# Optimization experiments

Measured on AMD Instinct MI355X. Metric: run time of the kernel, lower is better.

Reference implementation:

```python
import jax, jax.numpy as jnp
import numpy as np
import math

B, S, H = 2, 2048, 1024
NH, HD = 16, 64
MAX_SCALE = 4


def setup_inputs() -> dict:
    key = jax.random.key(0)
    ks = jax.random.split(key, 8)
    s = 0.02
    return {
        "x": jax.random.normal(ks[0], (B, S, H), dtype=jnp.float32),
        "Wqkv": jax.random.normal(ks[1], (H, 3 * H), dtype=jnp.float32) * s,
        "bqkv": jnp.zeros((3 * H,), dtype=jnp.float32),
        "Wout": jax.random.normal(ks[2], (H, H), dtype=jnp.float32) * s,
        "bout": jnp.zeros((H,), dtype=jnp.float32),
        "Wscale": jax.random.normal(ks[3], (H, MAX_SCALE), dtype=jnp.float32) * s,
        "bscale": jnp.zeros((MAX_SCALE,), dtype=jnp.float32),
    }


def reference(x, Wqkv, bqkv, Wout, bout, Wscale, bscale):
    b, s, h = x.shape
    inv_sqrt_hd = 1.0 / math.sqrt(HD)
    # qkv projection -> [3, b, nh, s, hd]
    qkv = (x @ Wqkv + bqkv).reshape(b, s, 3, NH, HD).transpose(2, 0, 3, 1, 4)
    q, k, v = qkv[0], qkv[1], qkv[2]
    # per-token soft weights over scales [b, s, max_scale]
    scale_weights = jax.nn.softmax(x @ Wscale + bscale, axis=-1)
    out = jnp.zeros((b, NH, s, HD), dtype=x.dtype)
    for scale_idx in range(MAX_SCALE):
        dilation = 2 ** scale_idx
        kd = k[:, :, ::dilation]  # strided (dilated) gather of keys
        vd = v[:, :, ::dilation]
        scores = jnp.einsum("bhqd,bhkd->bhqk", q, kd) * inv_sqrt_hd
        attn = jax.nn.softmax(scores, axis=-1)
        o = jnp.einsum("bhqk,bhkd->bhqd", attn, vd)
        w = scale_weights[:, :, scale_idx][:, None, :, None]  # [b,1,s,1]
        out = out + o * w
    out = out.transpose(0, 2, 1, 3).reshape(b, s, h)
    return out @ Wout + bout
```

## Files before the change

kernel.cpp:

```cpp
#include <hip/hip_runtime.h>
#include <stdint.h>

typedef unsigned short u16;
typedef __attribute__((ext_vector_type(8))) __bf16 bf8v;
typedef __attribute__((ext_vector_type(4))) float f4v;
typedef __attribute__((ext_vector_type(16))) float f16v;

#define BB 2
#define SS 2048
#define HH 1024

#define OFF_Q   0u
#define OFF_K0  8388608u
#define OFF_K1  16777216u
#define OFF_K2  20971520u
#define OFF_K3  23068672u
#define OFF_V0  24117248u
#define OFF_V1  32505856u
#define OFF_V2  36700160u
#define OFF_V3  38797312u
#define OFF_WQT 39845888u
#define OFF_WOT 46137344u
#define OFF_XB  48234496u
#define OFF_SCW 56623104u

__device__ __forceinline__ u16 f2bf(float f) {
    union { float f; uint32_t u; } v; v.f = f;
    uint32_t r = v.u + 0x7fffu + ((v.u >> 16) & 1u);
    return (u16)(r >> 16);
}
__device__ __forceinline__ uint32_t pk2(float a, float b) {
    return (uint32_t)f2bf(a) | ((uint32_t)f2bf(b) << 16);
}
__device__ __forceinline__ uint32_t pkt2(float a, float b) {
    union { float f; uint32_t u; } x, y; x.f = a; y.f = b;
    return (x.u >> 16) | (y.u & 0xffff0000u);
}
__device__ __forceinline__ u16 f2bft(float f) {
    union { float f; uint32_t u; } v; v.f = f;
    return (u16)(v.u >> 16);
}

__global__ __launch_bounds__(256) void xconv_kernel(const float* __restrict__ x,
                                                    u16* __restrict__ xb) {
    size_t t = (size_t)blockIdx.x * 256 + threadIdx.x;
    float4 v = *(const float4*)&x[t * 4];
    uint2 pk; pk.x = pk2(v.x, v.y); pk.y = pk2(v.z, v.w);
    *(uint2*)&xb[t * 4] = pk;
}

__global__ __launch_bounds__(256) void wconv_kernel(const float* __restrict__ W,
                                                    u16* __restrict__ Wt,
                                                    int N, int K) {
    __shared__ float tile[64][69];
    const int tid = threadIdx.x;
    const int n0 = blockIdx.x * 64, k0 = blockIdx.y * 64;
    const int r = tid >> 4, c4 = (tid & 15) * 4;
#pragma unroll
    for (int it = 0; it < 4; it++) {
        float4 v = *(const float4*)&W[(size_t)(k0 + it * 16 + r) * N + n0 + c4];
        tile[it * 16 + r][c4 + 0] = v.x; tile[it * 16 + r][c4 + 1] = v.y;
        tile[it * 16 + r][c4 + 2] = v.z; tile[it * 16 + r][c4 + 3] = v.w;
    }
    __syncthreads();
#pragma unroll
    for (int it = 0; it < 4; it++) {
        int n = it * 16 + r;
        uint2 pk;
        pk.x = pk2(tile[c4 + 0][n], tile[c4 + 1][n]);
        pk.y = pk2(tile[c4 + 2][n], tile[c4 + 3][n]);
        *(uint2*)&Wt[(size_t)(n0 + n) * K + k0 + c4] = pk;
    }
}

__global__ __launch_bounds__(256) void scale_kernel(const float* __restrict__ x,
                                                    const float* __restrict__ Wscale,
                                                    const float* __restrict__ bscale,
                                                    float* __restrict__ scw) {
    const int lane = threadIdx.x & 63;
    const int wid  = threadIdx.x >> 6;
    const int row  = blockIdx.x * 4 + wid;
    float a0 = 0.f, a1 = 0.f, a2 = 0.f, a3 = 0.f;
    for (int i = 0; i < 16; i++) {
        int hh = lane + i * 64;
        float xs = x[(size_t)row * HH + hh];
        float4 wv = *(const float4*)&Wscale[hh * 4];
        a0 += xs * wv.x; a1 += xs * wv.y; a2 += xs * wv.z; a3 += xs * wv.w;
    }
    for (int off = 1; off < 64; off <<= 1) {
        a0 += __shfl_xor(a0, off); a1 += __shfl_xor(a1, off);
        a2 += __shfl_xor(a2, off); a3 += __shfl_xor(a3, off);
    }
    if (lane == 0) {
        a0 += bscale[0]; a1 += bscale[1]; a2 += bscale[2]; a3 += bscale[3];
        float mx = fmaxf(fmaxf(a0, a1), fmaxf(a2, a3));
        float e0 = __expf(a0 - mx), e1 = __expf(a1 - mx);
        float e2 = __expf(a2 - mx), e3 = __expf(a3 - mx);
        float inv = 1.f / (e0 + e1 + e2 + e3);
        float4 o = {e0 * inv, e1 * inv, e2 * inv, e3 * inv};
        *(float4*)&scw[(size_t)row * 4] = o;
    }
}

template<int MODE>
__global__ __launch_bounds__(256) void gemm_bt(const u16* __restrict__ A,
                                               const u16* __restrict__ Bt,
                                               const float* __restrict__ bias,
                                               void* __restrict__ Cp,
                                               int N, int K) {
    __shared__ __align__(16) u16 At[128 * 40];
    __shared__ __align__(16) u16 Btl[128 * 40];
    const int tid  = threadIdx.x;
    const int lane = tid & 63;
    const int wid  = tid >> 6;
    const int l15  = lane & 15;
    const int quad = lane >> 4;
    const int wm = wid & 1, wn = wid >> 1;
    const int m0 = blockIdx.y * 128;
    const int n0 = blockIdx.x * 128;
    const int srow = tid >> 2;
    const int sc8  = (tid & 3) * 8;

    f4v acc[4][4];
#pragma unroll
    for (int i = 0; i < 4; i++)
#pragma unroll
        for (int j = 0; j < 4; j++) acc[i][j] = (f4v){0.f, 0.f, 0.f, 0.f};

    uint4 pa0 = *(const uint4*)(A  + (size_t)(m0 + srow) * K + sc8);
    uint4 pa1 = *(const uint4*)(A  + (size_t)(m0 + srow + 64) * K + sc8);
    uint4 pb0 = *(const uint4*)(Bt + (size_t)(n0 + srow) * K + sc8);
    uint4 pb1 = *(const uint4*)(Bt + (size_t)(n0 + srow + 64) * K + sc8);

    for (int kc = 0; kc < K; kc += 32) {
        __syncthreads();
        *(uint4*)&At[srow * 40 + sc8]         = pa0;
        *(uint4*)&At[(srow + 64) * 40 + sc8]  = pa1;
        *(uint4*)&Btl[srow * 40 + sc8]        = pb0;
        *(uint4*)&Btl[(srow + 64) * 40 + sc8] = pb1;
        __syncthreads();
        if (kc + 32 < K) {
            pa0 = *(const uint4*)(A  + (size_t)(m0 + srow) * K + kc + 32 + sc8);
            pa1 = *(const uint4*)(A  + (size_t)(m0 + srow + 64) * K + kc + 32 + sc8);
            pb0 = *(const uint4*)(Bt + (size_t)(n0 + srow) * K + kc + 32 + sc8);
            pb1 = *(const uint4*)(Bt + (size_t)(n0 + srow + 64) * K + kc + 32 + sc8);
        }
        bf8v af[4], bf[4];
#pragma unroll
        for (int t = 0; t < 4; t++) {
            af[t] = *(const bf8v*)&At[(wm * 64 + t * 16 + l15) * 40 + quad * 8];
            bf[t] = *(const bf8v*)&Btl[(wn * 64 + t * 16 + l15) * 40 + quad * 8];
        }
#pragma unroll
        for (int ti = 0; ti < 4; ti++)
#pragma unroll
            for (int tj = 0; tj < 4; tj++)
                acc[ti][tj] = __builtin_amdgcn_mfma_f32_16x16x32_bf16(af[ti], bf[tj], acc[ti][tj], 0, 0, 0);
    }

    if (MODE == 0) {
#pragma unroll
        for (int ti = 0; ti < 4; ti++)
#pragma unroll
            for (int tj = 0; tj < 4; tj++)
#pragma unroll
                for (int r = 0; r < 4; r++) {
                    int m = m0 + wm * 64 + ti * 16 + quad * 4 + r;
                    int n = n0 + wn * 64 + tj * 16 + l15;
                    ((float*)Cp)[(size_t)m * N + n] = acc[ti][tj][r] + bias[n];
                }
    } else {
        char* ws = (char*)Cp;
        u16* Qd = (u16*)ws;
        u16* K0 = (u16*)(ws + OFF_K0);
        u16* V0 = (u16*)(ws + OFF_V0); u16* V1 = (u16*)(ws + OFF_V1);
        u16* V2 = (u16*)(ws + OFF_V2); u16* V3 = (u16*)(ws + OFF_V3);
        const int region = n0 >> 10;
        if (region == 0) {
#pragma unroll
            for (int ti = 0; ti < 4; ti++)
#pragma unroll
                for (int tj = 0; tj < 4; tj++)
#pragma unroll
                    for (int r = 0; r < 4; r++) {
                        int m = m0 + wm * 64 + ti * 16 + quad * 4 + r;
                        int n = n0 + wn * 64 + tj * 16 + l15;
                        Qd[(size_t)m * 1024 + n] = f2bf(acc[ti][tj][r] + bias[n]);
                    }
        } else if (region == 1) {
#pragma unroll
            for (int ti = 0; ti < 4; ti++)
#pragma unroll
                for (int tj = 0; tj < 4; tj++) {
                    int n  = n0 + wn * 64 + tj * 16 + l15;
                    int nk = n - 1024;
                    int h = nk >> 6, hd = nk & 63;
#pragma unroll
                    for (int r = 0; r < 4; r++) {
                        int m = m0 + wm * 64 + ti * 16 + quad * 4 + r;
                        int bb = m >> 11, tok = m & 2047;
                        int bh = bb * 16 + h;
                        u16 bv = f2bf((acc[ti][tj][r] + bias[n]) * 0.18033688f);
                        K0[((size_t)bh * 2048 + tok) * 64 + hd] = bv;
                    }
                }
        } else {
#pragma unroll
            for (int ti = 0; ti < 4; ti++)
#pragma unroll
                for (int tj = 0; tj < 4; tj++) {
                    int n  = n0 + wn * 64 + tj * 16 + l15;
                    int nv = n - 2048;
                    int h = nv >> 6, hd = nv & 63;
                    int tokb = m0 + wm * 64 + ti * 16 + quad * 4;
                    int bb = tokb >> 11, tok = tokb & 2047;
                    int bh = bb * 16 + h;
                    float v0 = acc[ti][tj][0] + bias[n];
                    float v1 = acc[ti][tj][1] + bias[n];
                    float v2 = acc[ti][tj][2] + bias[n];
                    float v3 = acc[ti][tj][3] + bias[n];
                    u16 c0 = f2bf(v0), c1 = f2bf(v1), c2 = f2bf(v2), c3 = f2bf(v3);
                    uint2 pk;
                    pk.x = (uint32_t)c0 | ((uint32_t)c1 << 16);
                    pk.y = (uint32_t)c2 | ((uint32_t)c3 << 16);
                    *(uint2*)&V0[((size_t)bh * 64 + hd) * 2048 + tok] = pk;
                    *(uint32_t*)&V1[((size_t)bh * 64 + hd) * 1024 + (tok >> 1)] =
                        (uint32_t)c0 | ((uint32_t)c2 << 16);
                    V2[((size_t)bh * 64 + hd) * 512 + (tok >> 2)] = c0;
                    if (!(quad & 1)) V3[((size_t)bh * 64 + hd) * 256 + (tok >> 3)] = c0;
                }
        }
    }
}

__global__ __launch_bounds__(256, 2) void attn_kernel(const char* __restrict__ ws) {
    __shared__ __align__(16) u16 smem[30208];
    u16* Kt0  = smem;
    u16* Kt1  = smem + 2304;
    u16* Vt0  = smem + 4608;
    u16* Vt1  = smem + 7168;
    u16* V1t0 = smem + 9728;
    u16* V1t1 = smem + 11264;
    u16* V2t  = smem + 12800;
    u16* V3t  = smem + 14336;

    const u16* Qd    = (const u16*)(ws + OFF_Q);
    const float* scw = (const float*)(ws + OFF_SCW);
    u16* attnb       = (u16*)(ws + OFF_Q);

    const int tid  = threadIdx.x;
    const int lane = tid & 63;
    const int wid  = tid >> 6;
    const int l31  = lane & 31;
    const int half = lane >> 5;
    const int b = blockIdx.z, h = blockIdx.y;
    const int q  = blockIdx.x * 128 + wid * 32 + l31;
    const int bh = b * 16 + h;

    u16* Pw0 = smem + 15872 + wid * 3584;
    u16* Pwe = Pw0 + 1280;
    u16* Pw2 = Pwe + 768;
    u16* Pw3 = Pw2 + 768;

    const int skey = tid >> 3;
    const int shd8 = (tid & 7) * 8;
    const int svhd = tid >> 2;
    const int svk8 = (tid & 3) * 8;
    const int vi4  = (tid & 3) * 4;

    bf8v qf[4];
#pragma unroll
    for (int ks = 0; ks < 4; ks++)
        qf[ks] = *(const bf8v*)(Qd + (size_t)(b * SS + q) * 1024 + h * 64 + ks * 16 + half * 8);

    const u16* Kb  = (const u16*)(ws + OFF_K0) + (size_t)bh * (2048 * 64);
    const u16* Vb0 = (const u16*)(ws + OFF_V0) + (size_t)bh * (64 * 2048);
    const u16* Vb1 = (const u16*)(ws + OFF_V1) + (size_t)bh * (64 * 1024);
    const u16* Vb2 = (const u16*)(ws + OFF_V2) + (size_t)bh * (64 * 512);
    const u16* Vb3 = (const u16*)(ws + OFF_V3) + (size_t)bh * (64 * 256);

    f16v oacc0[2], oacc1[2], oacc2[2], oacc3[2];
#pragma unroll
    for (int ht = 0; ht < 2; ht++)
#pragma unroll
        for (int r = 0; r < 16; r++) {
            oacc0[ht][r] = 0.f; oacc1[ht][r] = 0.f;
            oacc2[ht][r] = 0.f; oacc3[ht][r] = 0.f;
        }
    float ls0 = 0.f, ls1 = 0.f, ls2 = 0.f, ls3 = 0.f;

    uint4 kr  = *(const uint4*)(Kb + (size_t)skey * 64 + shd8);
    uint4 vr  = *(const uint4*)(Vb0 + (size_t)svhd * 2048 + svk8);
    uint2 v1r = *(const uint2*)(Vb1 + (size_t)svhd * 1024 + vi4);
    uint2 v2r = *(const uint2*)(Vb2 + (size_t)svhd * 512 + vi4);
    uint2 v3r = *(const uint2*)(Vb3 + (size_t)svhd * 256 + vi4);
    *(uint4*)&Kt0[skey * 72 + shd8] = kr;
    *(uint4*)&Vt0[svhd * 40 + svk8] = vr;
    *(uint2*)&V1t0[svhd * 24 + vi4] = v1r;
    kr  = *(const uint4*)(Kb + (size_t)(32 + skey) * 64 + shd8);
    vr  = *(const uint4*)(Vb0 + (size_t)svhd * 2048 + 32 + svk8);
    v1r = *(const uint2*)(Vb1 + (size_t)svhd * 1024 + 16 + vi4);
    __syncthreads();

    for (int c = 0; c < 64; c++) {
        u16* Ktc  = (c & 1) ? Kt1 : Kt0;
        u16* Vtc  = (c & 1) ? Vt1 : Vt0;
        u16* V1tc = (c & 1) ? V1t1 : V1t0;
        u16* Ktn  = (c & 1) ? Kt0 : Kt1;
        u16* Vtn  = (c & 1) ? Vt0 : Vt1;
        u16* V1tn = (c & 1) ? V1t0 : V1t1;

        f16v sa;
#pragma unroll
        for (int r = 0; r < 16; r++) sa[r] = 0.f;
#pragma unroll
        for (int ks = 0; ks < 4; ks++) {
            bf8v ka = *(const bf8v*)&Ktc[l31 * 72 + ks * 16 + half * 8];
            sa = __builtin_amdgcn_mfma_f32_32x32x16_bf16(ka, qf[ks], sa, 0, 0, 0);
        }
#pragma unroll
        for (int g = 0; g < 4; g++) {
            float e0 = exp2f(sa[g * 4 + 0]);
            float e1 = exp2f(sa[g * 4 + 1]);
            float e2 = exp2f(sa[g * 4 + 2]);
            float e3 = exp2f(sa[g * 4 + 3]);
            ls0 += (e0 + e1) + (e2 + e3);
            ls1 += e0 + e2;
            ls2 += e0;
            if (!half) ls3 += e0;
            uint2 pk;
            pk.x = pkt2(e0, e1);
            pk.y = pkt2(e2, e3);
            *(uint2*)&Pw0[l31 * 40 + g * 8 + half * 4] = pk;
            *(uint32_t*)&Pwe[l31 * 24 + g * 4 + half * 2] = pkt2(e0, e2);
            Pw2[l31 * 24 + (c & 1) * 8 + g * 2 + half] = f2bft(e0);
            if (!half) Pw3[l31 * 24 + (c & 3) * 4 + g] = f2bft(e0);
        }
        if (c + 1 < 64) {
            *(uint4*)&Ktn[skey * 72 + shd8] = kr;
            *(uint4*)&Vtn[svhd * 40 + svk8] = vr;
            *(uint2*)&V1tn[svhd * 24 + vi4] = v1r;
        }
        if (!(c & 1)) {
            *(uint2*)&V2t[svhd * 24 + vi4] = v2r;
            if (!(c & 3))
                *(uint2*)&V3t[svhd * 24 + vi4] = v3r;
        }
        if (c + 2 < 64) {
            kr  = *(const uint4*)(Kb + (size_t)((c + 2) * 32 + skey) * 64 + shd8);
            vr  = *(const uint4*)(Vb0 + (size_t)svhd * 2048 + (c + 2) * 32 + svk8);
            v1r = *(const uint2*)(Vb1 + (size_t)svhd * 1024 + (c + 2) * 16 + vi4);
            if (!((c + 2) & 1))
                v2r = *(const uint2*)(Vb2 + (size_t)svhd * 512 + (c + 2) * 8 + vi4);
            if (!((c + 2) & 3))
                v3r = *(const uint2*)(Vb3 + (size_t)svhd * 256 + (c + 2) * 4 + vi4);
        }
        __asm__ volatile("s_waitcnt lgkmcnt(0)" ::: "memory");
#pragma unroll
        for (int kst = 0; kst < 2; kst++) {
            bf8v pb = *(const bf8v*)&Pw0[l31 * 40 + kst * 16 + half * 8];
#pragma unroll
            for (int ht = 0; ht < 2; ht++) {
                bf8v va = *(const bf8v*)&Vtc[(ht * 32 + l31) * 40 + kst * 16 + half * 8];
                oacc0[ht] = __builtin_amdgcn_mfma_f32_32x32x16_bf16(va, pb, oacc0[ht], 0, 0, 0);
            }
        }
        {
            bf8v pb1 = *(const bf8v*)&Pwe[l31 * 24 + half * 8];
#pragma unroll
            for (int ht = 0; ht < 2; ht++) {
                bf8v va1 = *(const bf8v*)&V1tc[(ht * 32 + l31) * 24 + half * 8];
                oacc1[ht] = __builtin_amdgcn_mfma_f32_32x32x16_bf16(va1, pb1, oacc1[ht], 0, 0, 0);
            }
        }
        if (c & 1) {
            bf8v pb2 = *(const bf8v*)&Pw2[l31 * 24 + half * 8];
#pragma unroll
            for (int ht = 0; ht < 2; ht++) {
                bf8v va2 = *(const bf8v*)&V2t[(ht * 32 + l31) * 24 + half * 8];
                oacc2[ht] = __builtin_amdgcn_mfma_f32_32x32x16_bf16(va2, pb2, oacc2[ht], 0, 0, 0);
            }
        }
        if ((c & 3) == 3) {
            bf8v pb3 = *(const bf8v*)&Pw3[l31 * 24 + half * 8];
#pragma unroll
            for (int ht = 0; ht < 2; ht++) {
                bf8v va3 = *(const bf8v*)&V3t[(ht * 32 + l31) * 24 + half * 8];
                oacc3[ht] = __builtin_amdgcn_mfma_f32_32x32x16_bf16(va3, pb3, oacc3[ht], 0, 0, 0);
            }
        }
        __syncthreads();
    }
    ls0 += __shfl_xor(ls0, 32);
    ls1 += __shfl_xor(ls1, 32);
    ls2 += __shfl_xor(ls2, 32);
    ls3 += __shfl_xor(ls3, 32);
    float4 sw = *(const float4*)&scw[(size_t)(b * SS + q) * 4];
    float w0 = sw.x / ls0, w1 = sw.y / ls1, w2 = sw.z / ls2, w3 = sw.w / ls3;

    const size_t base = (size_t)(b * SS + q) * 1024 + h * 64;
#pragma unroll
    for (int ht = 0; ht < 2; ht++)
#pragma unroll
        for (int g = 0; g < 4; g++) {
            float f0 = w0 * oacc0[ht][g * 4 + 0] + w1 * oacc1[ht][g * 4 + 0]
                     + w2 * oacc2[ht][g * 4 + 0] + w3 * oacc3[ht][g * 4 + 0];
            float f1 = w0 * oacc0[ht][g * 4 + 1] + w1 * oacc1[ht][g * 4 + 1]
                     + w2 * oacc2[ht][g * 4 + 1] + w3 * oacc3[ht][g * 4 + 1];
            float f2 = w0 * oacc0[ht][g * 4 + 2] + w1 * oacc1[ht][g * 4 + 2]
                     + w2 * oacc2[ht][g * 4 + 2] + w3 * oacc3[ht][g * 4 + 2];
            float f3 = w0 * oacc0[ht][g * 4 + 3] + w1 * oacc1[ht][g * 4 + 3]
                     + w2 * oacc2[ht][g * 4 + 3] + w3 * oacc3[ht][g * 4 + 3];
            uint2 pk;
            pk.x = pk2(f0, f1);
            pk.y = pk2(f2, f3);
            *(uint2*)&attnb[base + ht * 32 + g * 8 + half * 4] = pk;
        }
}

extern "C" void kernel_launch(void* const* d_in, const int* in_sizes, int n_in,
                              void* d_out, int out_size, void* d_ws, size_t ws_size,
                              hipStream_t stream) {
    const float* x      = (const float*)d_in[0];
    const float* Wqkv   = (const float*)d_in[1];
    const float* bqkv   = (const float*)d_in[2];
    const float* Wout   = (const float*)d_in[3];
    const float* bout   = (const float*)d_in[4];
    const float* Wscale = (const float*)d_in[5];
    const float* bscale = (const float*)d_in[6];
    float* out = (float*)d_out;

    char* ws = (char*)d_ws;
    u16*   wqt   = (u16*)(ws + OFF_WQT);
    u16*   wot   = (u16*)(ws + OFF_WOT);
    u16*   xb    = (u16*)(ws + OFF_XB);
    u16*   attnb = (u16*)(ws + OFF_Q);
    float* scw   = (float*)(ws + OFF_SCW);

    xconv_kernel<<<dim3(4096), dim3(256), 0, stream>>>(x, xb);
    wconv_kernel<<<dim3(48, 16), dim3(256), 0, stream>>>(Wqkv, wqt, 3072, 1024);
    wconv_kernel<<<dim3(16, 16), dim3(256), 0, stream>>>(Wout, wot, 1024, 1024);
    scale_kernel<<<dim3(1024), dim3(256), 0, stream>>>(x, Wscale, bscale, scw);
    gemm_bt<1><<<dim3(24, 32), dim3(256), 0, stream>>>(xb, wqt, bqkv, (void*)ws, 3072, 1024);
    attn_kernel<<<dim3(16, 16, 2), dim3(256), 0, stream>>>(ws);
    gemm_bt<0><<<dim3(8, 32), dim3(256), 0, stream>>>(attnb, wot, bout, (void*)out, 1024, 1024);
}
```

Measured before the change: 266.8 us.

## Keep softmax probabilities in registers by permuting V layout to match MFMA fragments

The probability tiles are no longer round-tripped through shared memory. The exp results are packed directly into bf16 MFMA B-operand registers. To make that legal, the QKV epilogue writes V0/V1/V2 with a permuted token order that matches the register fragment layout, and the scale-3 operand is assembled with a cross-half shuffle. The loop is unrolled by four so phase-dependent buffer choices become compile-time. This cuts LDS traffic and the lgkmcnt wait, and halves shared memory per block, which may raise occupancy. The cost is subtle index permutations that must match the MFMA lane mapping exactly.

```diff
diff --git a/kernel.cpp b/kernel.cpp
--- a/kernel.cpp
+++ b/kernel.cpp
@@ -5,6 +5,7 @@
 typedef __attribute__((ext_vector_type(8))) __bf16 bf8v;
 typedef __attribute__((ext_vector_type(4))) float f4v;
 typedef __attribute__((ext_vector_type(16))) float f16v;
+typedef __attribute__((ext_vector_type(4))) uint32_t u32x4;
 
 #define BB 2
 #define SS 2048
@@ -12,9 +13,6 @@
 
 #define OFF_Q   0u
 #define OFF_K0  8388608u
-#define OFF_K1  16777216u
-#define OFF_K2  20971520u
-#define OFF_K3  23068672u
 #define OFF_V0  24117248u
 #define OFF_V1  32505856u
 #define OFF_V2  36700160u
@@ -35,10 +33,6 @@
 __device__ __forceinline__ uint32_t pkt2(float a, float b) {
     union { float f; uint32_t u; } x, y; x.f = a; y.f = b;
     return (x.u >> 16) | (y.u & 0xffff0000u);
-}
-__device__ __forceinline__ u16 f2bft(float f) {
-    union { float f; uint32_t u; } v; v.f = f;
-    return (u16)(v.u >> 16);
 }
 
 __global__ __launch_bounds__(256) void xconv_kernel(const float* __restrict__ x,
@@ -223,10 +217,15 @@
                     uint2 pk;
                     pk.x = (uint32_t)c0 | ((uint32_t)c1 << 16);
                     pk.y = (uint32_t)c2 | ((uint32_t)c3 << 16);
-                    *(uint2*)&V0[((size_t)bh * 64 + hd) * 2048 + tok] = pk;
-                    *(uint32_t*)&V1[((size_t)bh * 64 + hd) * 1024 + (tok >> 1)] =
+                    int tokp = (tok & ~15) | ((tok & 4) << 1) | ((tok & 8) >> 1);
+                    *(uint2*)&V0[((size_t)bh * 64 + hd) * 2048 + tokp] = pk;
+                    int kk = tok >> 1;
+                    int v1p = (kk & ~15) | ((kk & 2) << 2) | ((kk & 12) >> 1);
+                    *(uint32_t*)&V1[((size_t)bh * 64 + hd) * 1024 + v1p] =
                         (uint32_t)c0 | ((uint32_t)c2 << 16);
-                    V2[((size_t)bh * 64 + hd) * 512 + (tok >> 2)] = c0;
+                    int t2 = tok >> 2;
+                    int v2i = (t2 & ~15) | ((t2 & 1) << 3) | ((t2 & 15) >> 1);
+                    V2[((size_t)bh * 64 + hd) * 512 + v2i] = c0;
                     if (!(quad & 1)) V3[((size_t)bh * 64 + hd) * 256 + (tok >> 3)] = c0;
                 }
         }
@@ -234,7 +233,7 @@
 }
 
 __global__ __launch_bounds__(256, 2) void attn_kernel(const char* __restrict__ ws) {
-    __shared__ __align__(16) u16 smem[30208];
+    __shared__ __align__(16) u16 smem[15872];
     u16* Kt0  = smem;
     u16* Kt1  = smem + 2304;
     u16* Vt0  = smem + 4608;
@@ -256,11 +255,6 @@
     const int b = blockIdx.z, h = blockIdx.y;
     const int q  = blockIdx.x * 128 + wid * 32 + l31;
     const int bh = b * 16 + h;
-
-    u16* Pw0 = smem + 15872 + wid * 3584;
-    u16* Pwe = Pw0 + 1280;
-    u16* Pw2 = Pwe + 768;
-    u16* Pw3 = Pw2 + 768;
 
     const int skey = tid >> 3;
     const int shd8 = (tid & 7) * 8;
@@ -302,94 +296,118 @@
     v1r = *(const uint2*)(Vb1 + (size_t)svhd * 1024 + 16 + vi4);
     __syncthreads();
 
-    for (int c = 0; c < 64; c++) {
-        u16* Ktc  = (c & 1) ? Kt1 : Kt0;
-        u16* Vtc  = (c & 1) ? Vt1 : Vt0;
-        u16* V1tc = (c & 1) ? V1t1 : V1t0;
-        u16* Ktn  = (c & 1) ? Kt0 : Kt1;
-        u16* Vtn  = (c & 1) ? Vt0 : Vt1;
-        u16* V1tn = (c & 1) ? V1t0 : V1t1;
-
-        f16v sa;
-#pragma unroll
-        for (int r = 0; r < 16; r++) sa[r] = 0.f;
-#pragma unroll
-        for (int ks = 0; ks < 4; ks++) {
-            bf8v ka = *(const bf8v*)&Ktc[l31 * 72 + ks * 16 + half * 8];
-            sa = __builtin_amdgcn_mfma_f32_32x32x16_bf16(ka, qf[ks], sa, 0, 0, 0);
-        }
-#pragma unroll
-        for (int g = 0; g < 4; g++) {
-            float e0 = exp2f(sa[g * 4 + 0]);
-            float e1 = exp2f(sa[g * 4 + 1]);
-            float e2 = exp2f(sa[g * 4 + 2]);
-            float e3 = exp2f(sa[g * 4 + 3]);
-            ls0 += (e0 + e1) + (e2 + e3);
-            ls1 += e0 + e2;
-            ls2 += e0;
-            if (!half) ls3 += e0;
-            uint2 pk;
-            pk.x = pkt2(e0, e1);
-            pk.y = pkt2(e2, e3);
-            *(uint2*)&Pw0[l31 * 40 + g * 8 + half * 4] = pk;
-            *(uint32_t*)&Pwe[l31 * 24 + g * 4 + half * 2] = pkt2(e0, e2);
-            Pw2[l31 * 24 + (c & 1) * 8 + g * 2 + half] = f2bft(e0);
-            if (!half) Pw3[l31 * 24 + (c & 3) * 4 + g] = f2bft(e0);
-        }
-        if (c + 1 < 64) {
-            *(uint4*)&Ktn[skey * 72 + shd8] = kr;
-            *(uint4*)&Vtn[svhd * 40 + svk8] = vr;
-            *(uint2*)&V1tn[svhd * 24 + vi4] = v1r;
-        }
-        if (!(c & 1)) {
-            *(uint2*)&V2t[svhd * 24 + vi4] = v2r;
-            if (!(c & 3))
-                *(uint2*)&V3t[svhd * 24 + vi4] = v3r;
-        }
-        if (c + 2 < 64) {
-            kr  = *(const uint4*)(Kb + (size_t)((c + 2) * 32 + skey) * 64 + shd8);
-            vr  = *(const uint4*)(Vb0 + (size_t)svhd * 2048 + (c + 2) * 32 + svk8);
-            v1r = *(const uint2*)(Vb1 + (size_t)svhd * 1024 + (c + 2) * 16 + vi4);
-            if (!((c + 2) & 1))
-                v2r = *(const uint2*)(Vb2 + (size_t)svhd * 512 + (c + 2) * 8 + vi4);
-            if (!((c + 2) & 3))
-                v3r = *(const uint2*)(Vb3 + (size_t)svhd * 256 + (c + 2) * 4 + vi4);
-        }
-        __asm__ volatile("s_waitcnt lgkmcnt(0)" ::: "memory");
-#pragma unroll
-        for (int kst = 0; kst < 2; kst++) {
-            bf8v pb = *(const bf8v*)&Pw0[l31 * 40 + kst * 16 + half * 8];
-#pragma unroll
-            for (int ht = 0; ht < 2; ht++) {
-                bf8v va = *(const bf8v*)&Vtc[(ht * 32 + l31) * 40 + kst * 16 + half * 8];
-                oacc0[ht] = __builtin_amdgcn_mfma_f32_32x32x16_bf16(va, pb, oacc0[ht], 0, 0, 0);
-            }
-        }
-        {
-            bf8v pb1 = *(const bf8v*)&Pwe[l31 * 24 + half * 8];
-#pragma unroll
-            for (int ht = 0; ht < 2; ht++) {
-                bf8v va1 = *(const bf8v*)&V1tc[(ht * 32 + l31) * 24 + half * 8];
-                oacc1[ht] = __builtin_amdgcn_mfma_f32_32x32x16_bf16(va1, pb1, oacc1[ht], 0, 0, 0);
-            }
-        }
-        if (c & 1) {
-            bf8v pb2 = *(const bf8v*)&Pw2[l31 * 24 + half * 8];
-#pragma unroll
-            for (int ht = 0; ht < 2; ht++) {
-                bf8v va2 = *(const bf8v*)&V2t[(ht * 32 + l31) * 24 + half * 8];
-                oacc2[ht] = __builtin_amdgcn_mfma_f32_32x32x16_bf16(va2, pb2, oacc2[ht], 0, 0, 0);
-            }
-        }
-        if ((c & 3) == 3) {
-            bf8v pb3 = *(const bf8v*)&Pw3[l31 * 24 + half * 8];
-#pragma unroll
-            for (int ht = 0; ht < 2; ht++) {
-                bf8v va3 = *(const bf8v*)&V3t[(ht * 32 + l31) * 24 + half * 8];
-                oacc3[ht] = __builtin_amdgcn_mfma_f32_32x32x16_bf16(va3, pb3, oacc3[ht], 0, 0, 0);
-            }
-        }
-        __syncthreads();
+    uint32_t Pa[4], Pb[4];
+    union uu { u32x4 u; bf8v b; };
+
+    for (int cc = 0; cc < 64; cc += 4) {
+#pragma unroll
+        for (int ph = 0; ph < 4; ph++) {
+            const int c = cc + ph;
+            u16* Ktc  = (ph & 1) ? Kt1 : Kt0;
+            u16* Vtc  = (ph & 1) ? Vt1 : Vt0;
+            u16* V1tc = (ph & 1) ? V1t1 : V1t0;
+            u16* Ktn  = (ph & 1) ? Kt0 : Kt1;
+            u16* Vtn  = (ph & 1) ? Vt0 : Vt1;
+            u16* V1tn = (ph & 1) ? V1t0 : V1t1;
+
+            f16v sa;
+#pragma unroll
+            for (int r = 0; r < 16; r++) sa[r] = 0.f;
+#pragma unroll
+            for (int ks = 0; ks < 4; ks++) {
+                bf8v ka = *(const bf8v*)&Ktc[l31 * 72 + ks * 16 + half * 8];
+                sa = __builtin_amdgcn_mfma_f32_32x32x16_bf16(ka, qf[ks], sa, 0, 0, 0);
+            }
+            float e[16];
+#pragma unroll
+            for (int g = 0; g < 4; g++) {
+                float e0 = exp2f(sa[g * 4 + 0]);
+                float e1 = exp2f(sa[g * 4 + 1]);
+                float e2 = exp2f(sa[g * 4 + 2]);
+                float e3 = exp2f(sa[g * 4 + 3]);
+                e[g * 4 + 0] = e0; e[g * 4 + 1] = e1;
+                e[g * 4 + 2] = e2; e[g * 4 + 3] = e3;
+                ls0 += (e0 + e1) + (e2 + e3);
+                ls1 += e0 + e2;
+                ls2 += e0;
+                if (!half) ls3 += e0;
+            }
+            uint32_t F00 = pkt2(e[0],  e[1]),  F01 = pkt2(e[2],  e[3]);
+            uint32_t F02 = pkt2(e[4],  e[5]),  F03 = pkt2(e[6],  e[7]);
+            uint32_t F10 = pkt2(e[8],  e[9]),  F11 = pkt2(e[10], e[11]);
+            uint32_t F12 = pkt2(e[12], e[13]), F13 = pkt2(e[14], e[15]);
+            uint32_t G0 = pkt2(e[0],  e[2]),   G1 = pkt2(e[4],  e[6]);
+            uint32_t G2 = pkt2(e[8],  e[10]),  G3 = pkt2(e[12], e[14]);
+            Pa[ph] = pkt2(e[0], e[4]);
+            Pb[ph] = pkt2(e[8], e[12]);
+
+            if (c + 1 < 64) {
+                *(uint4*)&Ktn[skey * 72 + shd8] = kr;
+                *(uint4*)&Vtn[svhd * 40 + svk8] = vr;
+                *(uint2*)&V1tn[svhd * 24 + vi4] = v1r;
+            }
+            if (!(ph & 1)) {
+                *(uint2*)&V2t[svhd * 24 + vi4] = v2r;
+                if (ph == 0)
+                    *(uint2*)&V3t[svhd * 24 + vi4] = v3r;
+            }
+            if (c + 2 < 64) {
+                kr  = *(const uint4*)(Kb + (size_t)((c + 2) * 32 + skey) * 64 + shd8);
+                vr  = *(const uint4*)(Vb0 + (size_t)svhd * 2048 + (c + 2) * 32 + svk8);
+                v1r = *(const uint2*)(Vb1 + (size_t)svhd * 1024 + (c + 2) * 16 + vi4);
+                if (!((c + 2) & 1))
+                    v2r = *(const uint2*)(Vb2 + (size_t)svhd * 512 + (c + 2) * 8 + vi4);
+                if (!((c + 2) & 3))
+                    v3r = *(const uint2*)(Vb3 + (size_t)svhd * 256 + (c + 2) * 4 + vi4);
+            }
+            {
+                uu p0; p0.u = (u32x4){F00, F01, F02, F03};
+#pragma unroll
+                for (int ht = 0; ht < 2; ht++) {
+                    bf8v va = *(const bf8v*)&Vtc[(ht * 32 + l31) * 40 + half * 8];
+                    oacc0[ht] = __builtin_amdgcn_mfma_f32_32x32x16_bf16(va, p0.b, oacc0[ht], 0, 0, 0);
+                }
+                uu p1; p1.u = (u32x4){F10, F11, F12, F13};
+#pragma unroll
+                for (int ht = 0; ht < 2; ht++) {
+                    bf8v va = *(const bf8v*)&Vtc[(ht * 32 + l31) * 40 + 16 + half * 8];
+                    oacc0[ht] = __builtin_amdgcn_mfma_f32_32x32x16_bf16(va, p1.b, oacc0[ht], 0, 0, 0);
+                }
+            }
+            {
+                uu ps; ps.u = (u32x4){G0, G1, G2, G3};
+#pragma unroll
+                for (int ht = 0; ht < 2; ht++) {
+                    bf8v va1 = *(const bf8v*)&V1tc[(ht * 32 + l31) * 24 + half * 8];
+                    oacc1[ht] = __builtin_amdgcn_mfma_f32_32x32x16_bf16(va1, ps.b, oacc1[ht], 0, 0, 0);
+                }
+            }
+            if (ph == 1 || ph == 3) {
+                uu p2; p2.u = (u32x4){Pa[ph - 1], Pb[ph - 1], Pa[ph], Pb[ph]};
+#pragma unroll
+                for (int ht = 0; ht < 2; ht++) {
+                    bf8v va2 = *(const bf8v*)&V2t[(ht * 32 + l31) * 24 + half * 8];
+                    oacc2[ht] = __builtin_amdgcn_mfma_f32_32x32x16_bf16(va2, p2.b, oacc2[ht], 0, 0, 0);
+                }
+            }
+            if (ph == 3) {
+                uint32_t t0 = __shfl_xor(Pa[2], 32);
+                uint32_t t1 = __shfl_xor(Pb[2], 32);
+                uint32_t t2 = __shfl_xor(Pa[3], 32);
+                uint32_t t3 = __shfl_xor(Pb[3], 32);
+                uint32_t w0 = half ? t0 : Pa[0];
+                uint32_t w1 = half ? t1 : Pb[0];
+                uint32_t w2 = half ? t2 : Pa[1];
+                uint32_t w3 = half ? t3 : Pb[1];
+                uu p3; p3.u = (u32x4){w0, w1, w2, w3};
+#pragma unroll
+                for (int ht = 0; ht < 2; ht++) {
+                    bf8v va3 = *(const bf8v*)&V3t[(ht * 32 + l31) * 24 + half * 8];
+                    oacc3[ht] = __builtin_amdgcn_mfma_f32_32x32x16_bf16(va3, p3.b, oacc3[ht], 0, 0, 0);
+                }
+            }
+            __syncthreads();
+        }
     }
     ls0 += __shfl_xor(ls0, 32);
     ls1 += __shfl_xor(ls1, 32);
```

Result: no change. 264.1 us (-1.0%).
